# Kernel optimization log

Measured on AMD Instinct MI355X. Metric: run time of the kernel, lower is better.

## Reference

```python
import jax, jax.numpy as jnp
from jax import lax
import numpy as np

TAU_R = 1.0
TAU_W = 5.0
W_MIN, W_MAX = 0.0, 0.05


def setup_inputs() -> dict:
    key = jax.random.key(0)
    ks = jax.random.split(key, 7)
    B, n_kc, n_mbon, n_fbn, n_ext, T = 48, 800, 20, 60, 2, 121
    n_dan = n_mbon
    n_recur = n_mbon + n_fbn + n_dan
    dt = 0.5
    sqrt2 = np.sqrt(2.0)
    # W_recur built per original init: per-block std sqrt(1/(sqrt2 * n_group))
    W_mbon = jax.random.normal(ks[0], (n_recur, n_mbon)) * np.sqrt(1.0 / (sqrt2 * n_mbon))
    W_fbn = jax.random.normal(ks[1], (n_recur, n_fbn)) * np.sqrt(1.0 / (sqrt2 * n_fbn))
    W_dan = jax.random.normal(ks[2], (n_recur, n_dan)) * np.sqrt(1.0 / (sqrt2 * n_dan))
    W_recur = jnp.concatenate([W_mbon, W_fbn, W_dan], axis=1).astype(jnp.float32)
    W_readout = (jax.random.normal(ks[3], (1, n_mbon)) / np.sqrt(float(n_mbon))).astype(jnp.float32)
    bias = jnp.full((n_recur,), 0.1, jnp.float32)
    W_ext = jax.random.normal(ks[4], (n_fbn, n_ext), jnp.float32)
    # sparse binary odor activity (f_ones = 0.1)
    r_kc = (jax.random.uniform(ks[5], (B, n_kc, T)) < 0.1).astype(jnp.float32)
    r_ext = jax.random.normal(ks[6], (B, n_ext, T), jnp.float32)
    time = jnp.arange(T, dtype=jnp.float32) * dt
    W_kc0 = jnp.full((B, n_mbon, n_kc), W_MAX, jnp.float32)  # W_kc_mbon_0
    wt0 = jnp.full((B, n_mbon, n_kc), W_MAX, jnp.float32)
    return {"r_kc": r_kc, "r_ext": r_ext, "time": time, "W_kc0": W_kc0,
            "wt0": wt0, "W_recur": W_recur, "W_readout": W_readout,
            "bias": bias, "W_ext": W_ext, "n_batch": B}


def reference(r_kc, r_ext, time, W_kc0, wt0, W_recur, W_readout, bias, W_ext, n_batch):
    n_mbon, n_kc = W_kc0.shape[1], W_kc0.shape[2]
    n_fbn = W_ext.shape[0]
    n_recur = W_recur.shape[0]
    n_dan = n_recur - n_mbon - n_fbn
    dt = time[1] - time[0]
    # n_hop == 0: DAN -> MBON weights zeroed (no knockouts)
    Wr = W_recur.at[:n_mbon, -n_dan:].set(0.0)
    # initial state: 0.1 everywhere, MBONs at 0
    r0 = jnp.full((n_batch, n_recur), 0.1, W_recur.dtype).at[:, :n_mbon].set(0.0)
    readout0 = r0[:, :n_mbon] @ W_readout.T  # [B, 1]
    readout0 = readout0[:, 0]
    rb_kc0 = r_kc[:, :, 0]
    rb_dan0 = r0[:, -n_dan:]
    # time-major driving inputs for the T-1 update steps
    xs = (jnp.moveaxis(r_kc, 2, 0)[:-1], jnp.moveaxis(r_ext, 2, 0)[:-1])

    def step(carry, x):
        r, W, wt, rb_kc, rb_dan = carry
        rkc_t, rext_t = x
        I_mbon = jnp.einsum('bmk,bk->bm', W, rkc_t)          # KC -> MBON via plastic W
        I_fbn = rext_t @ W_ext.T                              # context -> FBN
        I_tot = (jnp.zeros_like(r)
                 .at[:, :n_mbon].set(I_mbon)
                 .at[:, n_mbon:n_mbon + n_fbn].set(I_fbn))
        Wr_prod = r @ Wr.T                                    # 'bsr,br->bs'
        r_new = r + (-r + jax.nn.relu(Wr_prod + bias + I_tot)) * (dt / TAU_R)
        r_dan = r_new[:, -n_dan:]
        # eligibility traces (updated BEFORE computing dw, per wt_update)
        rb_kc_new = rb_kc + (rkc_t - rb_kc) * (dt / TAU_W)
        rb_dan_new = rb_dan + (r_dan - rb_dan) * (dt / TAU_W)
        # LTP - LTD plasticity (Eq 4)
        dw = (jnp.einsum('bd,bk->bdk', rb_dan_new, rkc_t)
              - jnp.einsum('bd,bk->bdk', r_dan, rb_kc_new))
        wt_new = wt + dw * dt
        W_new = jnp.clip(W + (-W + wt_new) * (dt / TAU_W), W_MIN, W_MAX)
        ro = (r_new[:, :n_mbon] @ W_readout.T)[:, 0]
        return (r_new, W_new, wt_new, rb_kc_new, rb_dan_new), (r_new, W_new, wt_new, ro)

    _, (rs, Ws, wts, ros) = lax.scan(step, (r0, W_kc0, wt0, rb_kc0, rb_dan0), xs)
    r_all = jnp.concatenate([r0[None], rs], axis=0)           # [T, B, n_recur]
    W_all = jnp.concatenate([W_kc0[None], Ws], axis=0)        # [T, B, n_mbon, n_kc]
    wt_all = jnp.concatenate([wt0[None], wts], axis=0)        # [T, B, n_mbon, n_kc]
    ro_all = jnp.concatenate([readout0[None], ros], axis=0)   # [T, B]
    return r_all, W_all, wt_all, ro_all
```

## Files before the change

kernel.cpp:

```cpp
#include <hip/hip_runtime.h>


#define NB   48
#define NK   800
#define NM   20
#define NF   60
#define NE   2
#define TT   121
#define NR   100
#define ND   20
#define NSTEP 120
#define SLAB (NB * NM * NK)

#define R_OFF   0
#define W_OFF   580800
#define WT_OFF  93508800
#define RO_OFF  186436800

typedef float f4 __attribute__((ext_vector_type(4)));

__global__ __launch_bounds__(640)
void rnn_dyn_kernel(const float* __restrict__ r_kc,
                    const float* __restrict__ r_ext,
                    const float* __restrict__ timev,
                    const float* __restrict__ W_kc0,
                    const float* __restrict__ wt0,
                    const float* __restrict__ W_recur,
                    const float* __restrict__ W_readout,
                    const float* __restrict__ bias,
                    const float* __restrict__ W_ext,
                    float* __restrict__ out)
{
    const int b   = blockIdx.x;
    const int tid = threadIdx.x;
    const int d   = tid >> 5;
    const int kg  = tid & 31;

    __shared__ __align__(16) float Wr_sh[NR * NR];
    __shared__ __align__(16) float rkc_sh[NK];
    __shared__ __align__(16) float vsh[NK];
    __shared__ float rsh[NR];
    __shared__ float rnew_sh[NR];
    __shared__ float bias_sh[NR];
    __shared__ float Imbon_sh[NM];
    __shared__ float rbdan_sh[ND];
    __shared__ float rdan_sh[ND];
    __shared__ float Wro_sh[NM];

    const float dt  = timev[1] - timev[0];
    const float dtw = dt * 0.2f;
    const float dtr = dt;

    for (int idx = tid; idx < NR * NR; idx += 640) {
        int i = idx / NR, j = idx - i * NR;
        float w = W_recur[idx];
        if (i < NM && j >= NR - ND) w = 0.f;
        Wr_sh[idx] = w;
    }
    if (tid < NR) {
        bias_sh[tid] = bias[tid];
        float r0 = (tid < NM) ? 0.f : 0.1f;
        rsh[tid] = r0;
        out[R_OFF + (size_t)b * NR + tid] = r0;
    }
    if (tid < NM) { Wro_sh[tid] = W_readout[tid]; rbdan_sh[tid] = 0.1f; }
    if (tid == 0) out[RO_OFF + b] = 0.f;

    float4 Wv[7], wtv[7], uv[7];
    const size_t rowbase = ((size_t)b * NM + d) * NK;
    #pragma unroll
    for (int j = 0; j < 7; ++j) {
        int k0 = 4 * kg + 128 * j;
        if (k0 < NK) {
            Wv[j]  = *(const float4*)(W_kc0 + rowbase + k0);
            wtv[j] = *(const float4*)(wt0   + rowbase + k0);
        }
    }
    __syncthreads();

    for (int t = 0; t < NSTEP; ++t) {
        for (int k = tid; k < NK; k += 640) {
            float u = r_kc[((size_t)b * NK + k) * TT + t];
            rkc_sh[k] = u;
            float vold = (t == 0) ? u : vsh[k];
            vsh[k] = vold + (u - vold) * dtw;
        }
        __syncthreads();

        float partial = 0.f;
        #pragma unroll
        for (int j = 0; j < 7; ++j) {
            int k0 = 4 * kg + 128 * j;
            if (k0 < NK) {
                uv[j] = *(const float4*)&rkc_sh[k0];
                partial += Wv[j].x * uv[j].x + Wv[j].y * uv[j].y
                         + Wv[j].z * uv[j].z + Wv[j].w * uv[j].w;
            }
        }
        partial += __shfl_xor(partial, 1);
        partial += __shfl_xor(partial, 2);
        partial += __shfl_xor(partial, 4);
        partial += __shfl_xor(partial, 8);
        partial += __shfl_xor(partial, 16);
        if (kg == 0) Imbon_sh[d] = partial;

        float wp = 0.f;
        if (tid < 4 * NR) {
            int i = tid >> 2, jg = tid & 3;
            const float* wr = Wr_sh + i * NR + jg * 25;
            const float* rr = rsh + jg * 25;
            #pragma unroll
            for (int j = 0; j < 25; ++j) wp += rr[j] * wr[j];
            wp += __shfl_xor(wp, 1);
            wp += __shfl_xor(wp, 2);
        }
        __syncthreads();

        if (tid < 4 * NR && (tid & 3) == 0) {
            int i = tid >> 2;
            float Itot;
            if (i < NM) {
                Itot = Imbon_sh[i];
            } else if (i < NM + NF) {
                float e0 = r_ext[((size_t)b * NE + 0) * TT + t];
                float e1 = r_ext[((size_t)b * NE + 1) * TT + t];
                Itot = e0 * W_ext[(i - NM) * NE + 0] + e1 * W_ext[(i - NM) * NE + 1];
            } else {
                Itot = 0.f;
            }
            float act = fmaxf(wp + bias_sh[i] + Itot, 0.f);
            float rn  = rsh[i] + (act - rsh[i]) * dtr;
            rnew_sh[i] = rn;
            out[R_OFF + ((size_t)(t + 1) * NB + b) * NR + i] = rn;
        }
        __syncthreads();

        if (tid < ND) {
            float rd = rnew_sh[NR - ND + tid];
            rdan_sh[tid] = rd;
            rbdan_sh[tid] += (rd - rbdan_sh[tid]) * dtw;
        }
        if (tid >= 128 && tid < 128 + NR) rsh[tid - 128] = rnew_sh[tid - 128];
        if (tid == 64) {
            float ro = 0.f;
            #pragma unroll
            for (int m = 0; m < NM; ++m) ro += rnew_sh[m] * Wro_sh[m];
            out[RO_OFF + (size_t)(t + 1) * NB + b] = ro;
        }
        __syncthreads();

        float a = rbdan_sh[d];
        float c = rdan_sh[d];
        #pragma unroll
        for (int j = 0; j < 7; ++j) {
            int k0 = 4 * kg + 128 * j;
            if (k0 < NK) {
                float4 v4 = *(const float4*)&vsh[k0];
                wtv[j].x += dt * (a * uv[j].x - c * v4.x);
                wtv[j].y += dt * (a * uv[j].y - c * v4.y);
                wtv[j].z += dt * (a * uv[j].z - c * v4.z);
                wtv[j].w += dt * (a * uv[j].w - c * v4.w);
                Wv[j].x = fminf(fmaxf(Wv[j].x + (wtv[j].x - Wv[j].x) * dtw, 0.f), 0.05f);
                Wv[j].y = fminf(fmaxf(Wv[j].y + (wtv[j].y - Wv[j].y) * dtw, 0.f), 0.05f);
                Wv[j].z = fminf(fmaxf(Wv[j].z + (wtv[j].z - Wv[j].z) * dtw, 0.f), 0.05f);
                Wv[j].w = fminf(fmaxf(Wv[j].w + (wtv[j].w - Wv[j].w) * dtw, 0.f), 0.05f);
            }
        }
        __syncthreads();
    }
}

__global__ __launch_bounds__(256)
void plasticity_kernel(const float* __restrict__ r_kc,
                       const float* __restrict__ timev,
                       const float* __restrict__ W_kc0,
                       const float* __restrict__ wt0,
                       float* out)
{
    const int bd  = blockIdx.x;
    const int b   = bd / NM;
    const int d   = bd - b * NM;
    const int tid = threadIdx.x;

    __shared__ float a_sh[NSTEP];
    __shared__ float c_sh[NSTEP];
    __shared__ __align__(16) float u_sh[8][NK + 4];

    const float dt  = timev[1] - timev[0];
    const float dtw = dt * 0.2f;

    if (tid < NSTEP)
        c_sh[tid] = out[R_OFF + ((size_t)(tid + 1) * NB + b) * NR + (NR - ND + d)];
    __syncthreads();
    if (tid == 0) {
        float a = 0.1f;
        for (int t = 0; t < NSTEP; ++t) { a += (c_sh[t] - a) * dtw; a_sh[t] = a; }
    }

    const size_t rowbase = ((size_t)b * NM + d) * NK;
    const int  k0  = 4 * tid;
    const bool act = (k0 < NK);
    f4 Wv = {0.f, 0.f, 0.f, 0.f}, wtv = Wv, v4 = Wv;
    if (act) {
        Wv  = *(const f4*)(W_kc0 + rowbase + k0);
        wtv = *(const f4*)(wt0   + rowbase + k0);
        __builtin_nontemporal_store(Wv,  (f4*)(out + W_OFF  + rowbase + k0));
        __builtin_nontemporal_store(wtv, (f4*)(out + WT_OFF + rowbase + k0));
    }
    __syncthreads();

    const float* ub = r_kc + (size_t)b * NK * TT;

    for (int ch = 0; ch < NSTEP / 8; ++ch) {
        const int t0 = 8 * ch;
        #pragma unroll
        for (int it = 0; it < (NK * 8) / 256; ++it) {
            int idx = tid + 256 * it;
            int k = idx >> 3, tt = idx & 7;
            u_sh[tt][k] = ub[(size_t)k * TT + t0 + tt];
        }
        __syncthreads();

        if (act) {
            #pragma unroll
            for (int tt = 0; tt < 8; ++tt) {
                const int t = t0 + tt;
                f4 u4 = *(const f4*)&u_sh[tt][k0];
                if (t == 0) {
                    v4 = u4;
                } else {
                    v4.x += (u4.x - v4.x) * dtw;
                    v4.y += (u4.y - v4.y) * dtw;
                    v4.z += (u4.z - v4.z) * dtw;
                    v4.w += (u4.w - v4.w) * dtw;
                }
                const float a = a_sh[t];
                const float c = c_sh[t];
                wtv.x += dt * (a * u4.x - c * v4.x);
                wtv.y += dt * (a * u4.y - c * v4.y);
                wtv.z += dt * (a * u4.z - c * v4.z);
                wtv.w += dt * (a * u4.w - c * v4.w);
                Wv.x = fminf(fmaxf(Wv.x + (wtv.x - Wv.x) * dtw, 0.f), 0.05f);
                Wv.y = fminf(fmaxf(Wv.y + (wtv.y - Wv.y) * dtw, 0.f), 0.05f);
                Wv.z = fminf(fmaxf(Wv.z + (wtv.z - Wv.z) * dtw, 0.f), 0.05f);
                Wv.w = fminf(fmaxf(Wv.w + (wtv.w - Wv.w) * dtw, 0.f), 0.05f);
                const size_t slab = (size_t)(t + 1) * SLAB;
                __builtin_nontemporal_store(Wv,  (f4*)(out + W_OFF  + slab + rowbase + k0));
                __builtin_nontemporal_store(wtv, (f4*)(out + WT_OFF + slab + rowbase + k0));
            }
        }
        __syncthreads();
    }
}

extern "C" void kernel_launch(void* const* d_in, const int* in_sizes, int n_in,
                              void* d_out, int out_size, void* d_ws, size_t ws_size,
                              hipStream_t stream) {
    const float* r_kc      = (const float*)d_in[0];
    const float* r_ext     = (const float*)d_in[1];
    const float* timev     = (const float*)d_in[2];
    const float* W_kc0     = (const float*)d_in[3];
    const float* wt0       = (const float*)d_in[4];
    const float* W_recur   = (const float*)d_in[5];
    const float* W_readout = (const float*)d_in[6];
    const float* bias      = (const float*)d_in[7];
    const float* W_ext     = (const float*)d_in[8];
    float* out = (float*)d_out;

    rnn_dyn_kernel<<<dim3(NB), dim3(640), 0, stream>>>(
        r_kc, r_ext, timev, W_kc0, wt0, W_recur, W_readout, bias, W_ext, out);
    plasticity_kernel<<<dim3(NB * NM), dim3(256), 0, stream>>>(
        r_kc, timev, W_kc0, wt0, out);
}
```

Baseline: 1.189 ms.

## Chunk r_kc loads by 8 timesteps and cut per-step barriers in recurrent kernel

The recurrent kernel now stages r_kc for 8 timesteps at a time into shared memory with a single barrier per chunk, instead of doing a strided global gather each step. Per-thread eligibility traces are kept in registers, and r is double-buffered so each step needs two barriers instead of four. r_ext and W_ext are cached in shared memory, and the W_recur stride is padded to reduce bank conflicts. This trims the serial latency of the recurrent kernel at the cost of more registers and shared memory. That kernel is only one part of the total; the plasticity kernel is unchanged.

Measured after the change: 1.104 ms. 1.08x faster.

```diff
diff --git a/kernel.cpp b/kernel.cpp
--- a/kernel.cpp
+++ b/kernel.cpp
@@ -16,6 +16,9 @@
 #define W_OFF   580800
 #define WT_OFF  93508800
 #define RO_OFF  186436800
+
+#define WRS  101
+#define UPAD 804
 
 typedef float f4 __attribute__((ext_vector_type(4)));
 
@@ -36,15 +39,13 @@
     const int d   = tid >> 5;
     const int kg  = tid & 31;
 
-    __shared__ __align__(16) float Wr_sh[NR * NR];
-    __shared__ __align__(16) float rkc_sh[NK];
-    __shared__ __align__(16) float vsh[NK];
-    __shared__ float rsh[NR];
-    __shared__ float rnew_sh[NR];
+    __shared__ __align__(16) float Wr_sh[NR * WRS];
+    __shared__ __align__(16) float ubuf[8][UPAD];
+    __shared__ float rsh[2][NR];
     __shared__ float bias_sh[NR];
     __shared__ float Imbon_sh[NM];
-    __shared__ float rbdan_sh[ND];
-    __shared__ float rdan_sh[ND];
+    __shared__ float rext_sh[NE][TT];
+    __shared__ float Wext_sh[NF * NE];
     __shared__ float Wro_sh[NM];
 
     const float dt  = timev[1] - timev[0];
@@ -55,22 +56,29 @@
         int i = idx / NR, j = idx - i * NR;
         float w = W_recur[idx];
         if (i < NM && j >= NR - ND) w = 0.f;
-        Wr_sh[idx] = w;
-    }
+        Wr_sh[i * WRS + j] = w;
+    }
+    for (int idx = tid; idx < NE * TT; idx += 640) {
+        int e = idx / TT, s = idx - e * TT;
+        rext_sh[e][s] = r_ext[((size_t)b * NE + e) * TT + s];
+    }
+    if (tid < NF * NE) Wext_sh[tid] = W_ext[tid];
     if (tid < NR) {
         bias_sh[tid] = bias[tid];
         float r0 = (tid < NM) ? 0.f : 0.1f;
-        rsh[tid] = r0;
+        rsh[0][tid] = r0;
         out[R_OFF + (size_t)b * NR + tid] = r0;
     }
-    if (tid < NM) { Wro_sh[tid] = W_readout[tid]; rbdan_sh[tid] = 0.1f; }
+    if (tid < NM) Wro_sh[tid] = W_readout[tid];
     if (tid == 0) out[RO_OFF + b] = 0.f;
 
-    float4 Wv[7], wtv[7], uv[7];
+    float4 Wv[7], wtv[7], uv[7], vv[7];
+    float rbdan = 0.1f;
     const size_t rowbase = ((size_t)b * NM + d) * NK;
     #pragma unroll
     for (int j = 0; j < 7; ++j) {
         int k0 = 4 * kg + 128 * j;
+        vv[j] = (float4){0.f, 0.f, 0.f, 0.f};
         if (k0 < NK) {
             Wv[j]  = *(const float4*)(W_kc0 + rowbase + k0);
             wtv[j] = *(const float4*)(wt0   + rowbase + k0);
@@ -78,95 +86,102 @@
     }
     __syncthreads();
 
-    for (int t = 0; t < NSTEP; ++t) {
-        for (int k = tid; k < NK; k += 640) {
-            float u = r_kc[((size_t)b * NK + k) * TT + t];
-            rkc_sh[k] = u;
-            float vold = (t == 0) ? u : vsh[k];
-            vsh[k] = vold + (u - vold) * dtw;
+    const float* ub = r_kc + (size_t)b * NK * TT;
+
+    for (int ch = 0; ch < NSTEP / 8; ++ch) {
+        const int t0 = 8 * ch;
+        #pragma unroll
+        for (int it = 0; it < (NK * 8) / 640; ++it) {
+            int idx = tid + 640 * it;
+            int k = idx >> 3, tt = idx & 7;
+            ubuf[tt][k] = ub[(size_t)k * TT + t0 + tt];
         }
         __syncthreads();
 
-        float partial = 0.f;
         #pragma unroll
-        for (int j = 0; j < 7; ++j) {
-            int k0 = 4 * kg + 128 * j;
-            if (k0 < NK) {
-                uv[j] = *(const float4*)&rkc_sh[k0];
-                partial += Wv[j].x * uv[j].x + Wv[j].y * uv[j].y
-                         + Wv[j].z * uv[j].z + Wv[j].w * uv[j].w;
-            }
-        }
-        partial += __shfl_xor(partial, 1);
-        partial += __shfl_xor(partial, 2);
-        partial += __shfl_xor(partial, 4);
-        partial += __shfl_xor(partial, 8);
-        partial += __shfl_xor(partial, 16);
-        if (kg == 0) Imbon_sh[d] = partial;
-
-        float wp = 0.f;
-        if (tid < 4 * NR) {
-            int i = tid >> 2, jg = tid & 3;
-            const float* wr = Wr_sh + i * NR + jg * 25;
-            const float* rr = rsh + jg * 25;
+        for (int tt = 0; tt < 8; ++tt) {
+            const int t   = t0 + tt;
+            const int cur = t & 1, nxt = cur ^ 1;
+
+            float partial = 0.f;
             #pragma unroll
-            for (int j = 0; j < 25; ++j) wp += rr[j] * wr[j];
-            wp += __shfl_xor(wp, 1);
-            wp += __shfl_xor(wp, 2);
-        }
-        __syncthreads();
-
-        if (tid < 4 * NR && (tid & 3) == 0) {
-            int i = tid >> 2;
-            float Itot;
-            if (i < NM) {
-                Itot = Imbon_sh[i];
-            } else if (i < NM + NF) {
-                float e0 = r_ext[((size_t)b * NE + 0) * TT + t];
-                float e1 = r_ext[((size_t)b * NE + 1) * TT + t];
-                Itot = e0 * W_ext[(i - NM) * NE + 0] + e1 * W_ext[(i - NM) * NE + 1];
-            } else {
-                Itot = 0.f;
-            }
-            float act = fmaxf(wp + bias_sh[i] + Itot, 0.f);
-            float rn  = rsh[i] + (act - rsh[i]) * dtr;
-            rnew_sh[i] = rn;
-            out[R_OFF + ((size_t)(t + 1) * NB + b) * NR + i] = rn;
-        }
-        __syncthreads();
-
-        if (tid < ND) {
-            float rd = rnew_sh[NR - ND + tid];
-            rdan_sh[tid] = rd;
-            rbdan_sh[tid] += (rd - rbdan_sh[tid]) * dtw;
-        }
-        if (tid >= 128 && tid < 128 + NR) rsh[tid - 128] = rnew_sh[tid - 128];
-        if (tid == 64) {
-            float ro = 0.f;
+            for (int j = 0; j < 7; ++j) {
+                int k0 = 4 * kg + 128 * j;
+                if (k0 < NK) {
+                    uv[j] = *(const float4*)&ubuf[tt][k0];
+                    if (t == 0) {
+                        vv[j] = uv[j];
+                    } else {
+                        vv[j].x += (uv[j].x - vv[j].x) * dtw;
+                        vv[j].y += (uv[j].y - vv[j].y) * dtw;
+                        vv[j].z += (uv[j].z - vv[j].z) * dtw;
+                        vv[j].w += (uv[j].w - vv[j].w) * dtw;
+                    }
+                    partial += Wv[j].x * uv[j].x + Wv[j].y * uv[j].y
+                             + Wv[j].z * uv[j].z + Wv[j].w * uv[j].w;
+                }
+            }
+            partial += __shfl_xor(partial, 1);
+            partial += __shfl_xor(partial, 2);
+            partial += __shfl_xor(partial, 4);
+            partial += __shfl_xor(partial, 8);
+            partial += __shfl_xor(partial, 16);
+            if (kg == 0) Imbon_sh[d] = partial;
+
+            float wp = 0.f;
+            if (tid < 4 * NR) {
+                int i = tid >> 2, jg = tid & 3;
+                const float* wr = Wr_sh + i * WRS + jg * 25;
+                const float* rr = &rsh[cur][jg * 25];
+                #pragma unroll
+                for (int j = 0; j < 25; ++j) wp += rr[j] * wr[j];
+                wp += __shfl_xor(wp, 1);
+                wp += __shfl_xor(wp, 2);
+            }
+            __syncthreads();
+
+            if (tid < 4 * NR && (tid & 3) == 0) {
+                int i = tid >> 2;
+                float Itot;
+                if (i < NM) {
+                    Itot = Imbon_sh[i];
+                } else if (i < NM + NF) {
+                    Itot = rext_sh[0][t] * Wext_sh[(i - NM) * NE + 0]
+                         + rext_sh[1][t] * Wext_sh[(i - NM) * NE + 1];
+                } else {
+                    Itot = 0.f;
+                }
+                float act = fmaxf(wp + bias_sh[i] + Itot, 0.f);
+                float rn  = rsh[cur][i] + (act - rsh[cur][i]) * dtr;
+                rsh[nxt][i] = rn;
+                out[R_OFF + ((size_t)(t + 1) * NB + b) * NR + i] = rn;
+            }
+            __syncthreads();
+
+            float c = rsh[nxt][NR - ND + d];
+            rbdan += (c - rbdan) * dtw;
+            float a = rbdan;
             #pragma unroll
-            for (int m = 0; m < NM; ++m) ro += rnew_sh[m] * Wro_sh[m];
-            out[RO_OFF + (size_t)(t + 1) * NB + b] = ro;
-        }
-        __syncthreads();
-
-        float a = rbdan_sh[d];
-        float c = rdan_sh[d];
-        #pragma unroll
-        for (int j = 0; j < 7; ++j) {
-            int k0 = 4 * kg + 128 * j;
-            if (k0 < NK) {
-                float4 v4 = *(const float4*)&vsh[k0];
-                wtv[j].x += dt * (a * uv[j].x - c * v4.x);
-                wtv[j].y += dt * (a * uv[j].y - c * v4.y);
-                wtv[j].z += dt * (a * uv[j].z - c * v4.z);
-                wtv[j].w += dt * (a * uv[j].w - c * v4.w);
-                Wv[j].x = fminf(fmaxf(Wv[j].x + (wtv[j].x - Wv[j].x) * dtw, 0.f), 0.05f);
-                Wv[j].y = fminf(fmaxf(Wv[j].y + (wtv[j].y - Wv[j].y) * dtw, 0.f), 0.05f);
-                Wv[j].z = fminf(fmaxf(Wv[j].z + (wtv[j].z - Wv[j].z) * dtw, 0.f), 0.05f);
-                Wv[j].w = fminf(fmaxf(Wv[j].w + (wtv[j].w - Wv[j].w) * dtw, 0.f), 0.05f);
-            }
-        }
-        __syncthreads();
+            for (int j = 0; j < 7; ++j) {
+                int k0 = 4 * kg + 128 * j;
+                if (k0 < NK) {
+                    wtv[j].x += dt * (a * uv[j].x - c * vv[j].x);
+                    wtv[j].y += dt * (a * uv[j].y - c * vv[j].y);
+                    wtv[j].z += dt * (a * uv[j].z - c * vv[j].z);
+                    wtv[j].w += dt * (a * uv[j].w - c * vv[j].w);
+                    Wv[j].x = fminf(fmaxf(Wv[j].x + (wtv[j].x - Wv[j].x) * dtw, 0.f), 0.05f);
+                    Wv[j].y = fminf(fmaxf(Wv[j].y + (wtv[j].y - Wv[j].y) * dtw, 0.f), 0.05f);
+                    Wv[j].z = fminf(fmaxf(Wv[j].z + (wtv[j].z - Wv[j].z) * dtw, 0.f), 0.05f);
+                    Wv[j].w = fminf(fmaxf(Wv[j].w + (wtv[j].w - Wv[j].w) * dtw, 0.f), 0.05f);
+                }
+            }
+            if (tid == 64) {
+                float ro = 0.f;
+                #pragma unroll
+                for (int m = 0; m < NM; ++m) ro += rsh[nxt][m] * Wro_sh[m];
+                out[RO_OFF + (size_t)(t + 1) * NB + b] = ro;
+            }
+        }
     }
 }
 
```
